# Performance work log

Measured on AMD Instinct MI355X. Metric: run time of the kernel, lower is better.

## Reference

```python
import jax, jax.numpy as jnp
import numpy as np

N_NODES = 10000
N_EDGES = 640000
D_IN = 128
D_OUT = 128


def setup_inputs() -> dict:
    key = jax.random.key(0)
    k1, k2, k3, k4 = jax.random.split(key, 4)
    x = jax.random.normal(k1, (N_NODES, D_IN), dtype=jnp.float32)
    # PyG GCNConv weight: [dim_out, dim_in] (glorot)
    W = jax.random.normal(k2, (D_OUT, D_IN), dtype=jnp.float32) * (1.0 / np.sqrt(D_IN))
    b = jnp.zeros((D_OUT,), dtype=jnp.float32)
    edge_weight = jax.random.uniform(k3, (N_EDGES,), dtype=jnp.float32)
    edge_index = jax.random.randint(k4, (2, N_EDGES), 0, N_NODES, dtype=jnp.int32)
    return {"x": x, "W": W, "b": b, "edge_weight": edge_weight, "edge_index": edge_index}


def reference(x, W, b, edge_weight, edge_index):
    N = x.shape[0]
    # --- add self loops (fill weight = 1.0), PyG default ---
    loops = jnp.arange(N, dtype=edge_index.dtype)
    src = jnp.concatenate([edge_index[0], loops])
    dst = jnp.concatenate([edge_index[1], loops])
    ew = jnp.concatenate([edge_weight, jnp.ones((N,), dtype=edge_weight.dtype)])
    # --- symmetric GCN normalization: deg from target index ---
    deg = jax.ops.segment_sum(ew, dst, num_segments=N)
    dinv = jnp.where(deg > 0, jax.lax.rsqrt(deg), 0.0)
    norm = dinv[src] * ew * dinv[dst]  # [E+N]
    # --- linear transform then gather-scale-scatter aggregation ---
    h = x @ W.T  # [N, D_OUT]
    msgs = h[src] * norm[:, None]  # [E+N, D_OUT]
    out = jax.ops.segment_sum(msgs, dst, num_segments=N)
    return out + b
```

## Files before the change

### kernel.cpp

```cpp
#include <hip/hip_runtime.h>

#define N_NODES 10000
#define N_EDGES 640000
#define D 128
#define CAP 128

typedef unsigned long long ull;
typedef unsigned short u16;
typedef unsigned int u32;

#define CHUNKS 128
#define EPC 5000
#define GEMM_NPB 32
#define GEMM_BLOCKS ((N_NODES + GEMM_NPB - 1) / GEMM_NPB)
#define SMEM_BYTES 40000

__device__ __forceinline__ u16 f2bf(float f) {
    unsigned u = __float_as_uint(f);
    unsigned r = (u + 0x7fffu + ((u >> 16) & 1u)) >> 16;
    return (u16)r;
}


__global__ void __launch_bounds__(256, 2) k_hist_gemm(
    const int* __restrict__ dst,
    u16* __restrict__ rank_local, u16* __restrict__ bbase, u32* __restrict__ gcnt,
    const float* __restrict__ x, const float* __restrict__ W,
    u16* __restrict__ h_bf)
{
    extern __shared__ char smem[];
    const int t = threadIdx.x;

    if (blockIdx.x < CHUNKS) {
        u32* hist = (u32*)smem;
        for (int i = t; i < N_NODES; i += 256) hist[i] = 0;
        __syncthreads();

        const int e0 = blockIdx.x * EPC;
        #pragma unroll
        for (int i = 0; i < 20; ++i) {
            int idx = i * 256 + t;
            if (idx < EPC) {
                int e = e0 + idx;
                u32 old = atomicAdd(&hist[dst[e]], 1u);
                rank_local[e] = (u16)old;
            }
        }
        __syncthreads();

        u16* brow = bbase + (size_t)blockIdx.x * N_NODES;
        for (int i = t; i < N_NODES; i += 256) {
            u32 c = hist[i];
            if (c) {
                u32 base = atomicAdd(&gcnt[i], c);
                brow[i] = (u16)base;
            }
        }
    } else {
        float* xs = (float*)smem;
        const int gb = blockIdx.x - CHUNKS;
        const int node0 = gb * GEMM_NPB;
        const int col = t & 127;
        const int half = t >> 7;

        #pragma unroll
        for (int r = 0; r < 16; ++r) {
            int row = half * 16 + r;
            int n = node0 + row;
            xs[row * D + col] = (n < N_NODES) ? x[n * D + col] : 0.0f;
        }
        __syncthreads();

        float acc[16];
        #pragma unroll
        for (int r = 0; r < 16; ++r) acc[r] = 0.0f;

        const float4* Wrow = (const float4*)&W[col * D];
        const float* xbase = &xs[half * 16 * D];
        for (int k4 = 0; k4 < D / 4; ++k4) {
            float4 w = Wrow[k4];
            int k = k4 * 4;
            #pragma unroll
            for (int r = 0; r < 16; ++r) {
                acc[r] += xbase[r * D + k + 0] * w.x;
                acc[r] += xbase[r * D + k + 1] * w.y;
                acc[r] += xbase[r * D + k + 2] * w.z;
                acc[r] += xbase[r * D + k + 3] * w.w;
            }
        }
        #pragma unroll
        for (int r = 0; r < 16; ++r) {
            int n = node0 + half * 16 + r;
            if (n < N_NODES) h_bf[n * D + col] = f2bf(acc[r]);
        }
    }
}


__global__ void k_fill(const int* __restrict__ src, const int* __restrict__ dst,
                       const float* __restrict__ ew,
                       const u16* __restrict__ rank_local, const u16* __restrict__ bbase,
                       ull* __restrict__ csr) {
    int e = blockIdx.x * blockDim.x + threadIdx.x;
    if (e >= N_EDGES) return;
    int s = src[e], d = dst[e];
    int bb = e / EPC;
    int pos = (int)bbase[(size_t)bb * N_NODES + d] + (int)rank_local[e];
    csr[(size_t)d * CAP + pos] = ((ull)__float_as_uint(ew[e]) << 32) | (unsigned)s;
}


__global__ void k_dinv(const u32* __restrict__ gcnt, const ull* __restrict__ csr,
                       float* __restrict__ dinv) {
    const int n = blockIdx.x * 4 + (threadIdx.x >> 6);
    const int lane = threadIdx.x & 63;
    if (n >= N_NODES) return;
    const int deg = (int)gcnt[n];
    const ull* bucket = csr + (size_t)n * CAP;
    float s = 0.f;
    for (int j = lane; j < deg; j += 64)
        s += __uint_as_float((u32)(bucket[j] >> 32));
    #pragma unroll
    for (int k = 1; k < 64; k <<= 1) s += __shfl_xor(s, k);
    if (lane == 0) dinv[n] = rsqrtf(1.0f + s);
}


__global__ void k_agg(const u32* __restrict__ gcnt, const ull* __restrict__ csr,
                      const u16* __restrict__ h_bf, const float* __restrict__ dinv,
                      const float* __restrict__ b, float* __restrict__ out) {
    const int n = blockIdx.x;
    const int tid = threadIdx.x;
    const int jj = tid >> 4;
    const int lane = tid & 15;
    __shared__ int   ssrc[CAP];
    __shared__ float snm[CAP];
    __shared__ float4 red[128][2];

    const int deg = (int)gcnt[n];
    const float dn = dinv[n];
    const ull* bucket = csr + (size_t)n * CAP;

    if (tid < deg) {
        ull v = bucket[tid];
        int s = (int)(unsigned)(v & 0xffffffffu);
        float w = __uint_as_float((u32)(v >> 32));
        ssrc[tid] = s;
        snm[tid] = dinv[s] * w * dn;
    }
    __syncthreads();

    float acc[8];
    #pragma unroll
    for (int k = 0; k < 8; ++k) acc[k] = 0.0f;

    for (int j = jj; j < deg; j += 8) {
        int s = ssrc[j];
        float nm = snm[j];
        union { float4 f4; unsigned u[4]; } uu;
        uu.f4 = *(const float4*)(h_bf + (size_t)s * D + lane * 8);
        #pragma unroll
        for (int k = 0; k < 4; ++k) {
            acc[2 * k]     += __uint_as_float(uu.u[k] << 16) * nm;
            acc[2 * k + 1] += __uint_as_float(uu.u[k] & 0xffff0000u) * nm;
        }
    }
    red[tid][0] = make_float4(acc[0], acc[1], acc[2], acc[3]);
    red[tid][1] = make_float4(acc[4], acc[5], acc[6], acc[7]);
    __syncthreads();

    if (tid < 16) {
        float r0[8];
        #pragma unroll
        for (int k = 0; k < 8; ++k) r0[k] = 0.0f;
        #pragma unroll
        for (int s = 0; s < 8; ++s) {
            float4 a = red[s * 16 + tid][0];
            float4 c = red[s * 16 + tid][1];
            r0[0] += a.x; r0[1] += a.y; r0[2] += a.z; r0[3] += a.w;
            r0[4] += c.x; r0[5] += c.y; r0[6] += c.z; r0[7] += c.w;
        }
        float s2 = dn * dn;
        union { float4 f4; unsigned u[4]; } hh;
        hh.f4 = *(const float4*)(h_bf + (size_t)n * D + tid * 8);
        float hv[8];
        #pragma unroll
        for (int k = 0; k < 4; ++k) {
            hv[2 * k]     = __uint_as_float(hh.u[k] << 16);
            hv[2 * k + 1] = __uint_as_float(hh.u[k] & 0xffff0000u);
        }
        const float4* b4 = (const float4*)(b + tid * 8);
        float4 b0 = b4[0], b1 = b4[1];
        float4 o0, o1;
        o0.x = r0[0] + hv[0] * s2 + b0.x;
        o0.y = r0[1] + hv[1] * s2 + b0.y;
        o0.z = r0[2] + hv[2] * s2 + b0.z;
        o0.w = r0[3] + hv[3] * s2 + b0.w;
        o1.x = r0[4] + hv[4] * s2 + b1.x;
        o1.y = r0[5] + hv[5] * s2 + b1.y;
        o1.z = r0[6] + hv[6] * s2 + b1.z;
        o1.w = r0[7] + hv[7] * s2 + b1.w;
        float4* o4 = (float4*)(out + (size_t)n * D + tid * 8);
        o4[0] = o0;
        o4[1] = o1;
    }
}


extern "C" void kernel_launch(void* const* d_in, const int* in_sizes, int n_in,
                              void* d_out, int out_size, void* d_ws, size_t ws_size,
                              hipStream_t stream) {
    const float* x  = (const float*)d_in[0];
    const float* W  = (const float*)d_in[1];
    const float* b  = (const float*)d_in[2];
    const float* ew = (const float*)d_in[3];
    const int* ei   = (const int*)d_in[4];
    const int* src = ei;
    const int* dst = ei + N_EDGES;
    float* out = (float*)d_out;

    char* ws = (char*)d_ws;
    u16*   rank_local = (u16*)(ws);
    u16*   bbase      = (u16*)(ws + 1280000);
    u32*   gcnt       = (u32*)(ws + 3840000);
    float* dinv       = (float*)(ws + 3880000);
    u16*   h_bf       = (u16*)(ws + 3920000);
    ull*   csr        = (ull*)(ws + 6480000);

    hipMemsetAsync(gcnt, 0, 40000, stream);
    k_hist_gemm<<<CHUNKS + GEMM_BLOCKS, 256, SMEM_BYTES, stream>>>(
        dst, rank_local, bbase, gcnt, x, W, h_bf);
    k_fill<<<(N_EDGES + 255) / 256, 256, 0, stream>>>(src, dst, ew, rank_local, bbase, csr);
    k_dinv<<<(N_NODES + 3) / 4, 256, 0, stream>>>(gcnt, csr, dinv);
    k_agg<<<N_NODES, 128, 0, stream>>>(gcnt, csr, h_bf, dinv, b, out);
}
```

Measured before the change: 128.2 us.

## Fuse CSR fill and degree into histogram kernel via packed 64-bit atomics

The histogram blocks now atomically add a packed 64-bit value per edge, holding the count in the upper 16 bits and the edge weight as 32.32 fixed point in the lower bits. Each block then reserves global slots and writes the CSR entries directly, which removes the separate fill and dinv kernels and the rank/bbase intermediate arrays. The aggregation kernel computes dinv on the fly from the packed sums. In exchange, local histogram shared memory doubles to 80KB, which may reduce occupancy, and weight sums now carry fixed-point rounding.

```diff
diff --git a/kernel.cpp b/kernel.cpp
--- a/kernel.cpp
+++ b/kernel.cpp
@@ -13,7 +13,8 @@
 #define EPC 5000
 #define GEMM_NPB 32
 #define GEMM_BLOCKS ((N_NODES + GEMM_NPB - 1) / GEMM_NPB)
-#define SMEM_BYTES 40000
+#define SMEM_BYTES 80000
+#define FRACM 0xffffffffffffull
 
 __device__ __forceinline__ u16 f2bf(float f) {
     unsigned u = __float_as_uint(f);
@@ -22,38 +23,54 @@
 }
 
 
-__global__ void __launch_bounds__(256, 2) k_hist_gemm(
-    const int* __restrict__ dst,
-    u16* __restrict__ rank_local, u16* __restrict__ bbase, u32* __restrict__ gcnt,
+__global__ void __launch_bounds__(256, 2) k_hist_fill_gemm(
+    const int* __restrict__ src, const int* __restrict__ dst,
+    const float* __restrict__ ew, ull* __restrict__ gpacked,
     const float* __restrict__ x, const float* __restrict__ W,
-    u16* __restrict__ h_bf)
+    u16* __restrict__ h_bf, ull* __restrict__ csr)
 {
     extern __shared__ char smem[];
     const int t = threadIdx.x;
 
     if (blockIdx.x < CHUNKS) {
-        u32* hist = (u32*)smem;
+        ull* hist = (ull*)smem;
         for (int i = t; i < N_NODES; i += 256) hist[i] = 0;
         __syncthreads();
 
         const int e0 = blockIdx.x * EPC;
+        u32 dlr[20];
         #pragma unroll
         for (int i = 0; i < 20; ++i) {
             int idx = i * 256 + t;
+            dlr[i] = 0xffffffffu;
             if (idx < EPC) {
                 int e = e0 + idx;
-                u32 old = atomicAdd(&hist[dst[e]], 1u);
-                rank_local[e] = (u16)old;
-            }
-        }
-        __syncthreads();
-
-        u16* brow = bbase + (size_t)blockIdx.x * N_NODES;
+                int d = dst[e];
+                ull add = (1ull << 48) | (ull)(ew[e] * 4294967296.0f);
+                ull old = atomicAdd(&hist[d], add);
+                dlr[i] = ((u32)d << 7) | (u32)((old >> 48) & 127u);
+            }
+        }
+        __syncthreads();
+
         for (int i = t; i < N_NODES; i += 256) {
-            u32 c = hist[i];
-            if (c) {
-                u32 base = atomicAdd(&gcnt[i], c);
-                brow[i] = (u16)base;
+            ull v = hist[i];
+            if (v) {
+                ull old = atomicAdd(&gpacked[i], v);
+                hist[i] = old >> 48;
+            }
+        }
+        __syncthreads();
+
+        #pragma unroll
+        for (int i = 0; i < 20; ++i) {
+            if (dlr[i] != 0xffffffffu) {
+                int e = e0 + i * 256 + t;
+                int d = (int)(dlr[i] >> 7);
+                int lr = (int)(dlr[i] & 127u);
+                int slot = (int)(u32)hist[d] + lr;
+                csr[(size_t)d * CAP + slot] =
+                    ((ull)__float_as_uint(ew[e]) << 32) | (unsigned)src[e];
             }
         }
     } else {
@@ -97,38 +114,9 @@
 }
 
 
-__global__ void k_fill(const int* __restrict__ src, const int* __restrict__ dst,
-                       const float* __restrict__ ew,
-                       const u16* __restrict__ rank_local, const u16* __restrict__ bbase,
-                       ull* __restrict__ csr) {
-    int e = blockIdx.x * blockDim.x + threadIdx.x;
-    if (e >= N_EDGES) return;
-    int s = src[e], d = dst[e];
-    int bb = e / EPC;
-    int pos = (int)bbase[(size_t)bb * N_NODES + d] + (int)rank_local[e];
-    csr[(size_t)d * CAP + pos] = ((ull)__float_as_uint(ew[e]) << 32) | (unsigned)s;
-}
-
-
-__global__ void k_dinv(const u32* __restrict__ gcnt, const ull* __restrict__ csr,
-                       float* __restrict__ dinv) {
-    const int n = blockIdx.x * 4 + (threadIdx.x >> 6);
-    const int lane = threadIdx.x & 63;
-    if (n >= N_NODES) return;
-    const int deg = (int)gcnt[n];
-    const ull* bucket = csr + (size_t)n * CAP;
-    float s = 0.f;
-    for (int j = lane; j < deg; j += 64)
-        s += __uint_as_float((u32)(bucket[j] >> 32));
-    #pragma unroll
-    for (int k = 1; k < 64; k <<= 1) s += __shfl_xor(s, k);
-    if (lane == 0) dinv[n] = rsqrtf(1.0f + s);
-}
-
-
-__global__ void k_agg(const u32* __restrict__ gcnt, const ull* __restrict__ csr,
-                      const u16* __restrict__ h_bf, const float* __restrict__ dinv,
-                      const float* __restrict__ b, float* __restrict__ out) {
+__global__ void k_agg(const ull* __restrict__ gpacked, const ull* __restrict__ csr,
+                      const u16* __restrict__ h_bf, const float* __restrict__ b,
+                      float* __restrict__ out) {
     const int n = blockIdx.x;
     const int tid = threadIdx.x;
     const int jj = tid >> 4;
@@ -137,16 +125,19 @@
     __shared__ float snm[CAP];
     __shared__ float4 red[128][2];
 
-    const int deg = (int)gcnt[n];
-    const float dn = dinv[n];
+    const ull gp = gpacked[n];
+    const int deg = (int)(gp >> 48);
+    const float dn = rsqrtf(1.0f + (float)(gp & FRACM) * 0x1p-32f);
     const ull* bucket = csr + (size_t)n * CAP;
 
     if (tid < deg) {
         ull v = bucket[tid];
         int s = (int)(unsigned)(v & 0xffffffffu);
         float w = __uint_as_float((u32)(v >> 32));
+        ull gs = gpacked[s];
+        float ds_ = rsqrtf(1.0f + (float)(gs & FRACM) * 0x1p-32f);
         ssrc[tid] = s;
-        snm[tid] = dinv[s] * w * dn;
+        snm[tid] = ds_ * w * dn;
     }
     __syncthreads();
 
@@ -220,17 +211,12 @@
     float* out = (float*)d_out;
 
     char* ws = (char*)d_ws;
-    u16*   rank_local = (u16*)(ws);
-    u16*   bbase      = (u16*)(ws + 1280000);
-    u32*   gcnt       = (u32*)(ws + 3840000);
-    float* dinv       = (float*)(ws + 3880000);
-    u16*   h_bf       = (u16*)(ws + 3920000);
-    ull*   csr        = (ull*)(ws + 6480000);
-
-    hipMemsetAsync(gcnt, 0, 40000, stream);
-    k_hist_gemm<<<CHUNKS + GEMM_BLOCKS, 256, SMEM_BYTES, stream>>>(
-        dst, rank_local, bbase, gcnt, x, W, h_bf);
-    k_fill<<<(N_EDGES + 255) / 256, 256, 0, stream>>>(src, dst, ew, rank_local, bbase, csr);
-    k_dinv<<<(N_NODES + 3) / 4, 256, 0, stream>>>(gcnt, csr, dinv);
-    k_agg<<<N_NODES, 128, 0, stream>>>(gcnt, csr, h_bf, dinv, b, out);
-}
+    ull*   gpacked = (ull*)(ws);
+    u16*   h_bf    = (u16*)(ws + 80000);
+    ull*   csr     = (ull*)(ws + 2640000);
+
+    hipMemsetAsync(gpacked, 0, 80000, stream);
+    k_hist_fill_gemm<<<CHUNKS + GEMM_BLOCKS, 256, SMEM_BYTES, stream>>>(
+        src, dst, ew, gpacked, x, W, h_bf, csr);
+    k_agg<<<N_NODES, 128, 0, stream>>>(gpacked, csr, h_bf, b, out);
+}
```

Result: faster. 122.8 us (-4.2%).
